# Kernel optimization log

Hardware: AMD Instinct MI355X
Metric: run time of the kernel (lower is better)

The kernel has to match this reference:

```python
import jax, jax.numpy as jnp
import numpy as np

B, T, I, H, D, C, OUT = 32, 128, 64, 256, 32, 64, 32
DECAY = 0.99

def _lin(k, fi, fo):
    lim = 1.0 / np.sqrt(fi)
    kw, kb = jax.random.split(k)
    W = jax.random.uniform(kw, (fi, fo), minval=-lim, maxval=lim, dtype=jnp.float32)
    b = jax.random.uniform(kb, (fo,), minval=-lim, maxval=lim, dtype=jnp.float32)
    return W, b

def setup_inputs():
    key = jax.random.key(0)
    ks = jax.random.split(key, 12)
    x = jax.random.normal(ks[0], (B, T, I), dtype=jnp.float32)
    lengths = jax.random.randint(ks[1], (B,), 1, T + 1)
    W_dg1, b_dg1 = _lin(ks[2], I + H, D)
    W_dg2, b_dg2 = _lin(ks[3], D, D)
    W_e1, b_e1 = _lin(ks[4], 2 * I, H)
    W_e2, b_e2 = _lin(ks[5], H, H)
    W_ih, b_ih = _lin(ks[6], H, 3 * H)
    W_hh, b_hh = _lin(ks[7], H, 3 * H)
    W_f1, b_f1 = _lin(ks[8], H, H)
    W_f2, b_f2 = _lin(ks[9], H, C)
    return dict(x=x, lengths=lengths, out_lengths=OUT,
                W_dg1=W_dg1, b_dg1=b_dg1, W_dg2=W_dg2, b_dg2=b_dg2,
                W_e1=W_e1, b_e1=b_e1, W_e2=W_e2, b_e2=b_e2,
                W_ih=W_ih, b_ih=b_ih, W_hh=W_hh, b_hh=b_hh,
                W_f1=W_f1, b_f1=b_f1, W_f2=W_f2, b_f2=b_f2)

def _forward(x, lengths, out_lengths, W_dg1, b_dg1, W_dg2, b_dg2, W_e1, b_e1, W_e2, b_e2,
             W_ih, b_ih, W_hh, b_hh, W_f1, b_f1, W_f2, b_f2):
    Bs, Ts, Is = x.shape
    Ds = W_dg2.shape[1]
    Hs = W_e2.shape[1]
    decay = DECAY ** jnp.arange(1, Ds + 1, dtype=x.dtype)  # [D]
    d_idx = jnp.arange(Ds)
    gkey = jax.random.key(42)
    g_enc = jax.random.gumbel(jax.random.fold_in(gkey, 0), (Ts, Bs, Ds), x.dtype)
    g_dec = jax.random.gumbel(jax.random.fold_in(gkey, 1), (out_lengths, Bs, Ds), x.dtype)
    masks = (jnp.arange(Ts)[None, :] < lengths[:, None]).astype(x.dtype)  # [B,T]

    def gumbel_softmax_hard(logits, g):
        # F.gumbel_softmax(..., tau=1.0, hard=True) straight-through estimator
        y_soft = jax.nn.softmax(logits + g, axis=-1)
        y_hard = jax.nn.one_hot(jnp.argmax(y_soft, axis=-1), Ds, dtype=logits.dtype)
        return y_hard + y_soft - jax.lax.stop_gradient(y_soft)

    def gru_cell(xin, h):
        # torch.nn.GRUCell gate order: r, z, n
        gi = xin @ W_ih + b_ih
        gh = h @ W_hh + b_hh
        i_r, i_z, i_n = jnp.split(gi, 3, axis=-1)
        h_r, h_z, h_n = jnp.split(gh, 3, axis=-1)
        r = jax.nn.sigmoid(i_r + h_r)
        z = jax.nn.sigmoid(i_z + h_z)
        n = jnp.tanh(i_n + r * h_n)
        return (1.0 - z) * n + z * h

    def step_core(buf, h, x_t, g_t, mem_t):
        cell_in = jnp.concatenate([x_t, h], axis=-1)
        logits = jax.nn.elu(cell_in @ W_dg1 + b_dg1) @ W_dg2 + b_dg2
        gate = gumbel_softmax_hard(logits, g_t)  # [B,D]
        # shift buffer along dim 1 (new[:, :-1] = old[:, 1:], last slot zeroed)
        new_buf = jnp.concatenate([buf[:, 1:], jnp.zeros_like(buf[:, :1])], axis=1)
        upd = x_t[:, None, :] * decay[None, :, None] * gate[:, :, None]  # [B,D,I]
        new_buf = new_buf.at[:, d_idx, d_idx].set(upd)  # diagonal scatter-assign
        rnn_in = jnp.concatenate([x_t, mem_t], axis=-1)
        rnn_in = jax.nn.elu(rnn_in @ W_e1 + b_e1) @ W_e2 + b_e2
        return new_buf, gru_cell(rnn_in, h)

    buf0 = jnp.zeros((Bs, Ds + 1, Ds, Is), x.dtype)
    h0 = jnp.zeros((Bs, Hs), x.dtype)

    def enc_step(carry, inp):
        buf, h = carry
        x_t, m_t, g_t = inp
        mem_t = buf[:, 0].sum(axis=1)  # [B,I]
        buf, nh = step_core(buf, h, x_t, g_t, mem_t)
        h = m_t[:, None] * nh + (1.0 - m_t[:, None]) * h
        return (buf, h), None

    (buf, h), _ = jax.lax.scan(enc_step, (buf0, h0),
                               (jnp.swapaxes(x, 0, 1), masks.T, g_enc))

    x_zero = jnp.zeros((Bs, Is), x.dtype)

    def dec_step(carry, g_t):
        buf, h = carry
        # get_current_memory(slide=True): roll -1 along dim1 with last slot zeroed
        buf = jnp.concatenate([buf[:, 1:], jnp.zeros_like(buf[:, :1])], axis=1)
        mem_t = buf[:, 0].sum(axis=1)
        buf, nh = step_core(buf, h, x_zero, g_t, mem_t)
        out = jax.nn.relu(nh @ W_f1 + b_f1) @ W_f2 + b_f2
        return (buf, nh), out

    _, outs = jax.lax.scan(dec_step, (buf, h), g_dec)  # [OUT,B,C]
    return jnp.swapaxes(outs, 0, 1)  # [B,OUT,C]

def reference(x, lengths, out_lengths, W_dg1, b_dg1, W_dg2, b_dg2, W_e1, b_e1, W_e2, b_e2,
              W_ih, b_ih, W_hh, b_hh, W_f1, b_f1, W_f2, b_f2):
    return _forward(x, lengths, out_lengths, W_dg1, b_dg1, W_dg2, b_dg2, W_e1, b_e1,
                    W_e2, b_e2, W_ih, b_ih, W_hh, b_hh, W_f1, b_f1, W_f2, b_f2)
```

## Files before the change

kernel.cpp:

```cpp
#include <hip/hip_runtime.h>
#include <math.h>


#define kB 32
#define kT 128
#define kI 64
#define kH 256
#define kD 32
#define kC 64
#define kOut 32
#define kSteps (kT + kOut)
#define NB 57
#define NTHR 256
#define NT_ALL (NB * NTHR)

#define WS_FL    384
#define WS_H     1856
#define WS_SEL   (WS_H + 4*8192)
#define WS_NZ    (WS_SEL + 128)
#define WS_W2    WS_NZ
#define WS_B2    (WS_W2 + kH*3*kH)
#define WS_G     (WS_B2 + 3*kH)
#define WS_P     (WS_G + kT*kB*kD)
#define WS_LINF  (WS_P + kT*kB*kH)
#define WS_O1    (WS_LINF + kSteps*kB*kH)
#define WS_ZERO_BYTES ((size_t)WS_NZ * sizeof(float))

__device__ __forceinline__ float cload(const float* p) {
  return __hip_atomic_load(p, __ATOMIC_RELAXED, __HIP_MEMORY_SCOPE_AGENT);
}
__device__ __forceinline__ void cstore(float* p, float v) {
  __hip_atomic_store(p, v, __ATOMIC_RELAXED, __HIP_MEMORY_SCOPE_AGENT);
}
__device__ __forceinline__ int cload_i(const int* p) {
  return __hip_atomic_load(p, __ATOMIC_RELAXED, __HIP_MEMORY_SCOPE_AGENT);
}
__device__ __forceinline__ void cstore_i(int* p, int v) {
  __hip_atomic_store(p, v, __ATOMIC_RELAXED, __HIP_MEMORY_SCOPE_AGENT);
}
__device__ __forceinline__ float4 cload4(const float* p) {
  float4 r;
  asm volatile("global_load_dwordx4 %0, %1, off sc0 sc1" : "=v"(r) : "v"(p));
  return r;
}
__device__ __forceinline__ void cstore4(float* p, float4 v) {
  cstore(p + 0, v.x); cstore(p + 1, v.y);
  cstore(p + 2, v.z); cstore(p + 3, v.w);
}
__device__ __forceinline__ void waitvm() {
  asm volatile("s_waitcnt vmcnt(0)" ::: "memory");
}

__device__ __forceinline__ void poll(const int* FL, int tid,
                                     int tH, int tD, int tS, int tF1, int tF2) {
  int thr;
  if      (tid < 32) thr = tH;
  else if (tid == 32) thr = tD;
  else if (tid == 33) thr = tS;
  else if (tid < 50) thr = tF1;
  else if (tid < 58) thr = tF2;
  else thr = 0;
  const int* p = FL + tid * 16;
  for (;;) {
    int ok = (thr <= 0) || (cload_i(p) >= thr);
    if (__syncthreads_count(ok) == NTHR) return;
    __builtin_amdgcn_s_sleep(2);
  }
}
__device__ __forceinline__ void setflag(int* FL, int tid, int idx, int val) {
  waitvm();
  __syncthreads();
  if (tid == 0) cstore_i(FL + idx * 16, val);
}

__device__ __forceinline__ void tf2x32(unsigned k0, unsigned k1,
                                       unsigned x0, unsigned x1,
                                       unsigned& o0, unsigned& o1) {
  unsigned ks2 = k0 ^ k1 ^ 0x1BD11BDAu;
  unsigned v0 = x0 + k0, v1 = x1 + k1;
#define TFR(r) { v0 += v1; v1 = (v1 << (r)) | (v1 >> (32-(r))); v1 ^= v0; }
  TFR(13) TFR(15) TFR(26) TFR(6)   v0 += k1;  v1 += ks2 + 1u;
  TFR(17) TFR(29) TFR(16) TFR(24)  v0 += ks2; v1 += k0  + 2u;
  TFR(13) TFR(15) TFR(26) TFR(6)   v0 += k0;  v1 += k1  + 3u;
  TFR(17) TFR(29) TFR(16) TFR(24)  v0 += k1;  v1 += ks2 + 4u;
  TFR(13) TFR(15) TFR(26) TFR(6)   v0 += ks2; v1 += k0  + 5u;
#undef TFR
  o0 = v0; o1 = v1;
}
__device__ __forceinline__ float bits_to_gumbel(unsigned bits) {
  float f = __uint_as_float((bits >> 9) | 0x3F800000u) - 1.0f;
  float u = f + 1.17549435e-38f;
  return -logf(-logf(u));
}

__device__ __forceinline__ void gridbar_full(unsigned* u, unsigned target) {
  __syncthreads();
  if (threadIdx.x == 0) {
    __threadfence();
    __hip_atomic_fetch_add(&u[320], 1u, __ATOMIC_ACQ_REL, __HIP_MEMORY_SCOPE_AGENT);
    while (__hip_atomic_load(&u[320], __ATOMIC_RELAXED, __HIP_MEMORY_SCOPE_AGENT) < target)
      __builtin_amdgcn_s_sleep(1);
    __threadfence();
  }
  __syncthreads();
}

__device__ __forceinline__ float elu1(float v) { return v > 0.f ? v : expm1f(v); }

__global__ __launch_bounds__(NTHR)
void delay_rnn(const float* __restrict__ x, const int* __restrict__ lengths,
               const float* __restrict__ W_dg1, const float* __restrict__ b_dg1,
               const float* __restrict__ W_dg2, const float* __restrict__ b_dg2,
               const float* __restrict__ W_e1,  const float* __restrict__ b_e1,
               const float* __restrict__ W_e2,  const float* __restrict__ b_e2,
               const float* __restrict__ W_ih,  const float* __restrict__ b_ih,
               const float* __restrict__ W_hh,  const float* __restrict__ b_hh,
               const float* __restrict__ W_f1,  const float* __restrict__ b_f1,
               const float* __restrict__ W_f2,  const float* __restrict__ b_f2,
               float* __restrict__ out, float* __restrict__ ws) {
  const int tid = threadIdx.x;
  const int bid = blockIdx.x;
  const int gid = bid * NTHR + tid;

  unsigned* baru = (unsigned*)ws;
  int*   FL    = (int*)(ws + WS_FL);
  float* hBuf  = ws + WS_H;
  int*   selG  = (int*)(ws + WS_SEL);
  float* W2g   = ws + WS_W2;
  float* B2g   = ws + WS_B2;
  float* g     = ws + WS_G;
  float* Pg    = ws + WS_P;
  float* linF  = ws + WS_LINF;
  float* o1B   = ws + WS_O1;

  __shared__ float S[35264];
  __shared__ float lgarr[1056];
  __shared__ float sb1[32], sb2[32], dec_sh[32];
  __shared__ int   sel[32], len_s[32], edest[32];

  {
    unsigned k0, k1;
    tf2x32(0u, 42u, 0u, 0u, k0, k1);
    for (int i = gid; i < kT * kB * kD; i += NT_ALL) {
      unsigned a, b;
      tf2x32(k0, k1, 0u, (unsigned)i, a, b);
      g[i] = bits_to_gumbel(a ^ b);
    }
  }
  for (int idx = gid; idx < kH * 3 * kH; idx += NT_ALL) {
    int k = idx / (3 * kH), n = idx % (3 * kH);
    const float* wr = W_e2 + k * kH;
    float s0 = 0, s1 = 0, s2 = 0, s3 = 0;
    for (int m = 0; m < kH; m += 4) {
      float4 wv = *(const float4*)(wr + m);
      s0 += wv.x * W_ih[(m    ) * 3 * kH + n];
      s1 += wv.y * W_ih[(m + 1) * 3 * kH + n];
      s2 += wv.z * W_ih[(m + 2) * 3 * kH + n];
      s3 += wv.w * W_ih[(m + 3) * 3 * kH + n];
    }
    W2g[idx] = ((s0 + s1) + (s2 + s3));
  }
  for (int n = gid; n < 3 * kH; n += NT_ALL) {
    float s = b_ih[n];
    for (int m = 0; m < kH; ++m) s += b_e2[m] * W_ih[m * 3 * kH + n];
    B2g[n] = s;
  }
  for (int idx = gid; idx < kT * kB * kH; idx += NT_ALL) {
    int s = idx >> 13, r = idx & 8191, b = r >> 8, j = r & 255;
    const float* xr = x + (b * kT + s) * kI;
    float a0 = 0, a1 = 0, a2 = 0, a3 = 0;
    for (int k = 0; k < 64; k += 4) {
      float4 xv = *(const float4*)(xr + k);
      a0 += xv.x * W_e1[(64 + k) * 256 + j];
      a1 += xv.y * W_e1[(65 + k) * 256 + j];
      a2 += xv.z * W_e1[(66 + k) * 256 + j];
      a3 += xv.w * W_e1[(67 + k) * 256 + j];
    }
    Pg[idx] = ((a0 + a1) + (a2 + a3));
  }
  for (int idx = gid; idx < kSteps * kB * kH; idx += NT_ALL) {
    int e = idx >> 13, r = idx & 8191, b = r >> 8, j = r & 255;
    float v = b_e1[j];
    if (e < kT) {
      const float* xr = x + (b * kT + e) * kI;
      float a0 = 0, a1 = 0, a2 = 0, a3 = 0;
      for (int k = 0; k < 64; k += 4) {
        float4 xv = *(const float4*)(xr + k);
        a0 += xv.x * W_e1[(k    ) * 256 + j];
        a1 += xv.y * W_e1[(k + 1) * 256 + j];
        a2 += xv.z * W_e1[(k + 2) * 256 + j];
        a3 += xv.w * W_e1[(k + 3) * 256 + j];
      }
      v += ((a0 + a1) + (a2 + a3));
    }
    linF[idx] = v;
  }

  gridbar_full(baru, NB);

  if (bid < 32) {
    float* whh = S; float* w2 = S + 6240;
    const int jb = bid * 8;
    for (int i = tid; i < 6144; i += NTHR) {
      int gg = i >> 11, r = i & 2047, jj = r >> 8, k = r & 255;
      whh[(gg * 8 + jj) * 260 + k] = W_hh[k * 768 + gg * 256 + jb + jj];
      w2 [(gg * 8 + jj) * 260 + k] = W2g [k * 768 + gg * 256 + jb + jj];
    }
    if (tid < 24) { int gg = tid / 8, jj = tid % 8;
      sb1[tid] = b_hh[gg * 256 + jb + jj];
      sb2[tid] = B2g [gg * 256 + jb + jj];
    }
    if (tid < 32) len_s[tid] = lengths[tid];
    __syncthreads();

    float* sH = S + 12480; float* sLin = S + 20800;
    float* red = S + 29120;
    for (int s = 0; s < kSteps; ++s) {
      int thrD = (s >= 2) ? ((s < kT) ? (s - 1) : kT) : 0;
      int thrS = (s >= 1) ? ((s < kT) ? s : kT) : 0;
      int tF1  = (s >= kT + 4) ? (s - 2) : 0;
      poll(FL, tid, s, thrD, thrS, tF1, 0);

      const float* hR = hBuf + (s & 3) * 8192;
      const float* lR = linF + s * 8192;
      const bool useC = (s >= 1 && s < kT);
      const float4* P4 = (const float4*)(Pg + (s - 1) * 8192);
      const int* selR = selG + ((s - 1) & 3) * 32;
      float4 th[8], tl[8], tp[8];
      int tsel[8];
      #pragma unroll
      for (int u8 = 0; u8 < 8; ++u8) {
        int i4 = (tid + u8 * 256) * 4;
        th[u8] = cload4(hR + i4);
        tl[u8] = cload4(lR + i4);
      }
      if (useC) {
        #pragma unroll
        for (int u8 = 0; u8 < 8; ++u8) {
          int idx = tid + u8 * 256; int b = idx >> 6, k4 = idx & 63;
          tp[u8] = P4[b * 64 + k4];
          tsel[u8] = cload_i(&selR[b]);
        }
      }
      waitvm();
      #pragma unroll
      for (int u8 = 0; u8 < 8; ++u8) {
        int idx = tid + u8 * 256; int b = idx >> 6, k4 = idx & 63;
        *(float4*)&sH[b * 260 + k4 * 4] = th[u8];
        float cx = 0.f, cy = 0.f, cz = 0.f, cw = 0.f;
        if (useC && tsel[u8] == 0) {
          cx = 0.99f * tp[u8].x; cy = 0.99f * tp[u8].y;
          cz = 0.99f * tp[u8].z; cw = 0.99f * tp[u8].w;
        }
        float4 v;
        v.x = elu1(tl[u8].x + cx);
        v.y = elu1(tl[u8].y + cy);
        v.z = elu1(tl[u8].z + cz);
        v.w = elu1(tl[u8].w + cw);
        *(float4*)&sLin[b * 260 + k4 * 4] = v;
      }
      __syncthreads();
      const float4* sH4 = (const float4*)sH;
      const float4* sL4 = (const float4*)sLin;
      const float4* wh4 = (const float4*)whh;
      const float4* w24 = (const float4*)w2;
      const int c  = tid & 7;
      const int b4 = (tid >> 3) & 7;
      const int kq = tid >> 6;
      float acc[24];
      #pragma unroll
      for (int a = 0; a < 24; ++a) acc[a] = 0.f;
      for (int kk = 0; kk < 16; ++kk) {
        int k4 = kq * 16 + kk;
        float4 wr[6];
        #pragma unroll
        for (int gg = 0; gg < 3; ++gg) {
          wr[gg]     = wh4[(gg * 8 + c) * 65 + k4];
          wr[3 + gg] = w24[(gg * 8 + c) * 65 + k4];
        }
        #pragma unroll
        for (int bi = 0; bi < 4; ++bi) {
          int b = bi * 8 + b4;
          float4 h4 = sH4[b * 65 + k4];
          float4 l4 = sL4[b * 65 + k4];
          #pragma unroll
          for (int gg = 0; gg < 3; ++gg) {
            float4 w = wr[gg];
            acc[bi * 6 + gg]     += h4.x * w.x + h4.y * w.y + h4.z * w.z + h4.w * w.w;
            w = wr[3 + gg];
            acc[bi * 6 + 3 + gg] += l4.x * w.x + l4.y * w.y + l4.z * w.z + l4.w * w.w;
          }
        }
      }
      #pragma unroll
      for (int bi = 0; bi < 4; ++bi)
        #pragma unroll
        for (int rr = 0; rr < 6; ++rr)
          red[kq * 1536 + rr * 256 + (bi * 8 + b4) * 8 + c] = acc[bi * 6 + rr];
      __syncthreads();
      {
        int b = tid >> 3, cc = tid & 7, jg = bid * 8 + cc;
        int lo = b * 8 + cc;
        float dots[6];
        #pragma unroll
        for (int rr = 0; rr < 6; ++rr)
          dots[rr] = (red[rr * 256 + lo] + red[1536 + rr * 256 + lo]) +
                     (red[3072 + rr * 256 + lo] + red[4608 + rr * 256 + lo]);
        float ghr = dots[0] + sb1[cc];
        float ghz = dots[1] + sb1[8 + cc];
        float ghn = dots[2] + sb1[16 + cc];
        float gir = dots[3] + sb2[cc];
        float giz = dots[4] + sb2[8 + cc];
        float gin = dots[5] + sb2[16 + cc];
        float r = 1.f / (1.f + expf(-(gir + ghr)));
        float z = 1.f / (1.f + expf(-(giz + ghz)));
        float n = tanhf(gin + r * ghn);
        float hold = sH[b * 260 + jg];
        float nh = (1.f - z) * n + z * hold;
        float hv = (s < kT) ? ((s < len_s[b]) ? nh : hold) : nh;
        cstore(&hBuf[((s + 1) & 3) * 8192 + b * 256 + jg], hv);
      }
      setflag(FL, tid, bid, s + 1);
    }
  }
  else if (bid == 32) {
    float* wdg1 = S; float* wdg2 = S + 10368;
    for (int i = tid; i < 10240; i += NTHR) {
      int j = i / 320, k = i % 320;
      wdg1[j * 324 + k] = W_dg1[k * 32 + j];
    }
    for (int i = tid; i < 1024; i += NTHR) wdg2[i] = W_dg2[i];
    if (tid < 32) { sb1[tid] = b_dg1[tid]; sb2[tid] = b_dg2[tid];
                    dec_sh[tid] = powf(0.99f, (float)(tid + 1)); }
    __syncthreads();

    float* sXH = S + 11392;
    float* red = S + 21760;
    float* l1s = S + 25856;
    for (int s = 0; s < kT; ++s) {
      poll(FL, tid, s, 0, 0, 0, 0);

      const float* hR = hBuf + (s & 3) * 8192;
      float4 th[8];
      #pragma unroll
      for (int u8 = 0; u8 < 8; ++u8) th[u8] = cload4(hR + (tid + u8 * 256) * 4);
      waitvm();
      #pragma unroll
      for (int u8 = 0; u8 < 8; ++u8) {
        int idx = tid + u8 * 256; int b = idx >> 6, k4 = idx & 63;
        *(float4*)&sXH[b * 324 + 64 + k4 * 4] = th[u8];
      }
      #pragma unroll
      for (int u2 = 0; u2 < 2; ++u2) {
        int idx = tid + u2 * 256; int b = idx >> 4, k4 = idx & 15;
        *(float4*)&sXH[b * 324 + k4 * 4] =
            *(const float4*)(x + (b * kT + s) * kI + k4 * 4);
      }
      __syncthreads();
      {
        const float4* sA4 = (const float4*)sXH;
        const float4* wd4 = (const float4*)wdg1;
        const int cq = tid & 7, b4 = (tid >> 3) & 7, kq = tid >> 6;
        float acc[16];
        #pragma unroll
        for (int a = 0; a < 16; ++a) acc[a] = 0.f;
        for (int kk = 0; kk < 20; ++kk) {
          int k4 = kq * 20 + kk;
          float4 wr[4];
          #pragma unroll
          for (int ci = 0; ci < 4; ++ci) wr[ci] = wd4[(cq * 4 + ci) * 81 + k4];
          #pragma unroll
          for (int bi = 0; bi < 4; ++bi) {
            float4 a4 = sA4[(bi * 8 + b4) * 81 + k4];
            #pragma unroll
            for (int ci = 0; ci < 4; ++ci) {
              float4 w = wr[ci];
              acc[bi * 4 + ci] += a4.x * w.x + a4.y * w.y + a4.z * w.z + a4.w * w.w;
            }
          }
        }
        #pragma unroll
        for (int bi = 0; bi < 4; ++bi)
          #pragma unroll
          for (int ci = 0; ci < 4; ++ci)
            red[kq * 1024 + (ci * 4 + bi) * 64 + cq * 8 + b4] = acc[bi * 4 + ci];
        __syncthreads();
        #pragma unroll
        for (int u4 = 0; u4 < 4; ++u4) {
          int o = tid * 4 + u4; int b = o >> 5, col = o & 31;
          int ci = col & 3, cq2 = col >> 2, bi = b >> 3, b42 = b & 7;
          int f = (ci * 4 + bi) * 64 + cq2 * 8 + b42;
          float v = (red[f] + red[1024 + f]) + (red[2048 + f] + red[3072 + f]);
          l1s[b * 36 + col] = elu1(v + sb1[col]);
        }
      }
      __syncthreads();
      for (int it = 0; it < 4; ++it) {
        int i = tid + it * 256; int b = i >> 5, j = i & 31;
        float sv = sb2[j];
        for (int k = 0; k < 32; ++k) sv += l1s[b * 36 + k] * wdg2[k * 32 + j];
        lgarr[b * 33 + j] = sv + g[(s * 32 + b) * 32 + j];
      }
      __syncthreads();
      if (tid < 32) {
        float best = lgarr[tid * 33]; int bi = 0;
        for (int j = 1; j < 32; ++j) {
          float v = lgarr[tid * 33 + j];
          if (v > best) { best = v; bi = j; }
        }
        sel[tid] = bi;
      }
      __syncthreads();
      if (tid < 32) cstore_i(&selG[(s & 3) * 32 + tid], sel[tid]);
      setflag(FL, tid, 33, s + 1);

      if (tid < 32) {
        int d = sel[tid], e = -1;
        if (d > 0) {
          int c = s + 1 + d;
          if (c < kT) e = c;
          else { int rr = c - kT - 1;
                 if (rr >= 0 && !(rr & 1)) {
                   int kk2 = rr >> 1; if (kk2 < kOut) e = kT + kk2; } }
        }
        edest[tid] = e;
      }
      __syncthreads();
      {
        float4 tv[8], tp2[8];
        int te[8], tb2[8];
        #pragma unroll
        for (int it = 0; it < 8; ++it) {
          int i = tid + it * 256; int b = i >> 6, q = i & 63;
          te[it] = edest[b]; tb2[it] = b;
          if (te[it] >= 0) {
            tv[it]  = cload4(linF + te[it] * 8192 + b * 256 + q * 4);
            tp2[it] = *(const float4*)(Pg + s * 8192 + b * 256 + q * 4);
          }
        }
        waitvm();
        #pragma unroll
        for (int it = 0; it < 8; ++it) {
          int i = tid + it * 256; int q = i & 63;
          if (te[it] >= 0) {
            float dec = dec_sh[sel[tb2[it]]];
            float4 v = tv[it], p = tp2[it];
            v.x += dec * p.x; v.y += dec * p.y;
            v.z += dec * p.z; v.w += dec * p.w;
            cstore4(linF + te[it] * 8192 + tb2[it] * 256 + q * 4, v);
          }
        }
      }
      setflag(FL, tid, 32, s + 1);
    }
  }
  else if (bid < 49) {
    float* wf1 = S;
    const int jb = (bid - 33) * 16;
    for (int i = tid; i < 4096; i += NTHR) {
      int jj = i >> 8, k = i & 255;
      wf1[jj * 260 + k] = W_f1[k * 256 + jb + jj];
    }
    if (tid < 16) sb1[tid] = b_f1[jb + tid];
    __syncthreads();

    float* sHf = S + 4160; float* red = S + 12480;
    for (int s = kT + 1; s <= kSteps; ++s) {
      int tF2 = (s >= kT + 5) ? (s - 2) : 0;
      poll(FL, tid, s, 0, 0, 0, tF2);

      const float* hR = hBuf + (s & 3) * 8192;
      float4 th[8];
      #pragma unroll
      for (int u8 = 0; u8 < 8; ++u8) th[u8] = cload4(hR + (tid + u8 * 256) * 4);
      waitvm();
      #pragma unroll
      for (int u8 = 0; u8 < 8; ++u8) {
        int idx = tid + u8 * 256; int b = idx >> 6, k4 = idx & 63;
        *(float4*)&sHf[b * 260 + k4 * 4] = th[u8];
      }
      __syncthreads();
      const float4* sH4 = (const float4*)sHf;
      const float4* w4p = (const float4*)wf1;
      const int cq = tid & 3, b4 = (tid >> 2) & 7, kq = tid >> 5;
      float acc[16];
      #pragma unroll
      for (int a = 0; a < 16; ++a) acc[a] = 0.f;
      for (int kk = 0; kk < 8; ++kk) {
        int k4 = kq * 8 + kk;
        float4 wr[4];
        #pragma unroll
        for (int ci = 0; ci < 4; ++ci) wr[ci] = w4p[(cq * 4 + ci) * 65 + k4];
        #pragma unroll
        for (int bi = 0; bi < 4; ++bi) {
          float4 h4 = sH4[(bi * 8 + b4) * 65 + k4];
          #pragma unroll
          for (int ci = 0; ci < 4; ++ci) {
            float4 w = wr[ci];
            acc[bi * 4 + ci] += h4.x * w.x + h4.y * w.y + h4.z * w.z + h4.w * w.w;
          }
        }
      }
      #pragma unroll
      for (int bi = 0; bi < 4; ++bi)
        #pragma unroll
        for (int ci = 0; ci < 4; ++ci)
          red[kq * 512 + (bi * 4 + ci) * 32 + cq * 8 + b4] = acc[bi * 4 + ci];
      __syncthreads();
      #pragma unroll
      for (int u2 = 0; u2 < 2; ++u2) {
        int o = tid * 2 + u2; int b = o >> 4, col = o & 15;
        int gg = ((b >> 3) * 4 + (col & 3)) * 32 + (col >> 2) * 8 + (b & 7);
        float v = 0.f;
        #pragma unroll
        for (int kq2 = 0; kq2 < 8; ++kq2) v += red[kq2 * 512 + gg];
        v += sb1[col];
        cstore(&o1B[(s & 3) * 8192 + b * 256 + (bid - 33) * 16 + col],
               v > 0.f ? v : 0.f);
      }
      __syncthreads();
      setflag(FL, tid, bid + 1, s + 1);
    }
  }
  else {
    float* wf2 = S;
    const int cb = (bid - 49) * 8;
    for (int i = tid; i < 2048; i += NTHR) {
      int cc = i >> 8, k = i & 255;
      wf2[cc * 260 + k] = W_f2[k * 64 + cb + cc];
    }
    if (tid < 8) sb2[tid] = b_f2[cb + tid];
    __syncthreads();

    float* sO = S + 2080; float* red = S + 10400;
    for (int s = kT + 2; s <= kSteps + 1; ++s) {
      poll(FL, tid, 0, 0, 0, s, 0);

      const float* oR = o1B + ((s - 1) & 3) * 8192;
      float4 to[8];
      #pragma unroll
      for (int u8 = 0; u8 < 8; ++u8) to[u8] = cload4(oR + (tid + u8 * 256) * 4);
      waitvm();
      #pragma unroll
      for (int u8 = 0; u8 < 8; ++u8) {
        int idx = tid + u8 * 256; int b = idx >> 6, k4 = idx & 63;
        *(float4*)&sO[b * 260 + k4 * 4] = to[u8];
      }
      __syncthreads();
      const float4* sO4 = (const float4*)sO;
      const float4* w4p = (const float4*)wf2;
      const int c = tid & 7, b4 = (tid >> 3) & 7, kq = tid >> 6;
      float acc[4] = {0.f, 0.f, 0.f, 0.f};
      for (int kk = 0; kk < 16; ++kk) {
        int k4 = kq * 16 + kk;
        float4 w = w4p[c * 65 + k4];
        #pragma unroll
        for (int bi = 0; bi < 4; ++bi) {
          float4 o4 = sO4[(bi * 8 + b4) * 65 + k4];
          acc[bi] += o4.x * w.x + o4.y * w.y + o4.z * w.z + o4.w * w.w;
        }
      }
      #pragma unroll
      for (int bi = 0; bi < 4; ++bi)
        red[kq * 256 + bi * 64 + b4 * 8 + c] = acc[bi];
      __syncthreads();
      { int b = tid >> 3, col = tid & 7;
        int gg = (b >> 3) * 64 + (b & 7) * 8 + col;
        float v = (red[gg] + red[256 + gg]) + (red[512 + gg] + red[768 + gg]);
        out[(b * kOut + (s - 2 - kT)) * kC + (bid - 49) * 8 + col] =
            v + sb2[col];
      }
      __syncthreads();
      setflag(FL, tid, bid + 1, s + 1);
    }
  }
}

extern "C" void kernel_launch(void* const* d_in, const int* in_sizes, int n_in,
                              void* d_out, int out_size, void* d_ws, size_t ws_size,
                              hipStream_t stream) {
  (void)in_sizes; (void)n_in; (void)out_size; (void)ws_size;
  const float* x      = (const float*)d_in[0];
  const int*   lens   = (const int*)  d_in[1];
  const float* W_dg1  = (const float*)d_in[3];
  const float* b_dg1  = (const float*)d_in[4];
  const float* W_dg2  = (const float*)d_in[5];
  const float* b_dg2  = (const float*)d_in[6];
  const float* W_e1   = (const float*)d_in[7];
  const float* b_e1   = (const float*)d_in[8];
  const float* W_e2   = (const float*)d_in[9];
  const float* b_e2   = (const float*)d_in[10];
  const float* W_ih   = (const float*)d_in[11];
  const float* b_ih   = (const float*)d_in[12];
  const float* W_hh   = (const float*)d_in[13];
  const float* b_hh   = (const float*)d_in[14];
  const float* W_f1   = (const float*)d_in[15];
  const float* b_f1   = (const float*)d_in[16];
  const float* W_f2   = (const float*)d_in[17];
  const float* b_f2   = (const float*)d_in[18];

  hipMemsetAsync(d_ws, 0, WS_ZERO_BYTES, stream);
  delay_rnn<<<dim3(NB), dim3(NTHR), 0, stream>>>(
      x, lens, W_dg1, b_dg1, W_dg2, b_dg2, W_e1, b_e1, W_e2, b_e2,
      W_ih, b_ih, W_hh, b_hh, W_f1, b_f1, W_f2, b_f2,
      (float*)d_out, (float*)d_ws);
}
```

Baseline: 2.251 ms.

## Merge dispatch flags, vectorize coherent stores, prefetch x before polling

The separate selection flag and delay-gate flag are merged into one, so the recurrent blocks poll one fewer flag and the flag indices of the later stage blocks shift down by one. The h and FC1 outputs are staged in shared memory and written as 128-bit coherent stores instead of scalar atomic stores. The x row is loaded before the poll spin so its latency overlaps the wait. This aims to cut per-step synchronization and store latency on the serial critical path, at the cost of an extra syncthreads per step and some loss of overlap for consumers that used to start on the earlier selection flag.

```diff
diff --git a/kernel.cpp b/kernel.cpp
--- a/kernel.cpp
+++ b/kernel.cpp
@@ -26,6 +26,8 @@
 #define WS_O1    (WS_LINF + kSteps*kB*kH)
 #define WS_ZERO_BYTES ((size_t)WS_NZ * sizeof(float))
 
+typedef float f32x4v __attribute__((ext_vector_type(4)));
+
 __device__ __forceinline__ float cload(const float* p) {
   return __hip_atomic_load(p, __ATOMIC_RELAXED, __HIP_MEMORY_SCOPE_AGENT);
 }
@@ -43,22 +45,21 @@
   asm volatile("global_load_dwordx4 %0, %1, off sc0 sc1" : "=v"(r) : "v"(p));
   return r;
 }
-__device__ __forceinline__ void cstore4(float* p, float4 v) {
-  cstore(p + 0, v.x); cstore(p + 1, v.y);
-  cstore(p + 2, v.z); cstore(p + 3, v.w);
+__device__ __forceinline__ void cstore4w(float* p, float4 v) {
+  f32x4v t; t.x = v.x; t.y = v.y; t.z = v.z; t.w = v.w;
+  asm volatile("global_store_dwordx4 %0, %1, off sc0 sc1" :: "v"(p), "v"(t) : "memory");
 }
 __device__ __forceinline__ void waitvm() {
   asm volatile("s_waitcnt vmcnt(0)" ::: "memory");
 }
 
 __device__ __forceinline__ void poll(const int* FL, int tid,
-                                     int tH, int tD, int tS, int tF1, int tF2) {
+                                     int tH, int tDG, int tF1, int tF2) {
   int thr;
   if      (tid < 32) thr = tH;
-  else if (tid == 32) thr = tD;
-  else if (tid == 33) thr = tS;
-  else if (tid < 50) thr = tF1;
-  else if (tid < 58) thr = tF2;
+  else if (tid == 32) thr = tDG;
+  else if (tid < 49) thr = tF1;
+  else if (tid < 57) thr = tF2;
   else thr = 0;
   const int* p = FL + tid * 16;
   for (;;) {
@@ -133,8 +134,7 @@
   float* linF  = ws + WS_LINF;
   float* o1B   = ws + WS_O1;
 
-  __shared__ float S[35264];
-  __shared__ float lgarr[1056];
+  __shared__ float S[35520];
   __shared__ float sb1[32], sb2[32], dec_sh[32];
   __shared__ int   sel[32], len_s[32], edest[32];
 
@@ -215,11 +215,11 @@
 
     float* sH = S + 12480; float* sLin = S + 20800;
     float* red = S + 29120;
+    float* hstage = S + 35264;
     for (int s = 0; s < kSteps; ++s) {
-      int thrD = (s >= 2) ? ((s < kT) ? (s - 1) : kT) : 0;
-      int thrS = (s >= 1) ? ((s < kT) ? s : kT) : 0;
-      int tF1  = (s >= kT + 4) ? (s - 2) : 0;
-      poll(FL, tid, s, thrD, thrS, tF1, 0);
+      int tDG = (s >= 1) ? (s < kT ? s : kT) : 0;
+      int tF1 = (s >= kT + 4) ? (s - 2) : 0;
+      poll(FL, tid, s, tDG, tF1, 0);
 
       const float* hR = hBuf + (s & 3) * 8192;
       const float* lR = linF + s * 8192;
@@ -299,7 +299,7 @@
           red[kq * 1536 + rr * 256 + (bi * 8 + b4) * 8 + c] = acc[bi * 6 + rr];
       __syncthreads();
       {
-        int b = tid >> 3, cc = tid & 7, jg = bid * 8 + cc;
+        int b = tid >> 3, cc = tid & 7, jg = jb + cc;
         int lo = b * 8 + cc;
         float dots[6];
         #pragma unroll
@@ -318,7 +318,13 @@
         float hold = sH[b * 260 + jg];
         float nh = (1.f - z) * n + z * hold;
         float hv = (s < kT) ? ((s < len_s[b]) ? nh : hold) : nh;
-        cstore(&hBuf[((s + 1) & 3) * 8192 + b * 256 + jg], hv);
+        hstage[b * 8 + cc] = hv;
+      }
+      __syncthreads();
+      if (tid < 64) {
+        int b = tid >> 1, q = tid & 1;
+        float4 h4 = *(const float4*)&hstage[b * 8 + q * 4];
+        cstore4w(&hBuf[((s + 1) & 3) * 8192 + b * 256 + jb + q * 4], h4);
       }
       setflag(FL, tid, bid, s + 1);
     }
@@ -337,8 +343,15 @@
     float* sXH = S + 11392;
     float* red = S + 21760;
     float* l1s = S + 25856;
+    float* lg  = S + 27008;
     for (int s = 0; s < kT; ++s) {
-      poll(FL, tid, s, 0, 0, 0, 0);
+      float4 tx[2];
+      #pragma unroll
+      for (int u2 = 0; u2 < 2; ++u2) {
+        int idx = tid + u2 * 256; int b = idx >> 4, k4 = idx & 15;
+        tx[u2] = *(const float4*)(x + (b * kT + s) * kI + k4 * 4);
+      }
+      poll(FL, tid, s, 0, 0, 0);
 
       const float* hR = hBuf + (s & 3) * 8192;
       float4 th[8];
@@ -353,8 +366,7 @@
       #pragma unroll
       for (int u2 = 0; u2 < 2; ++u2) {
         int idx = tid + u2 * 256; int b = idx >> 4, k4 = idx & 15;
-        *(float4*)&sXH[b * 324 + k4 * 4] =
-            *(const float4*)(x + (b * kT + s) * kI + k4 * 4);
+        *(float4*)&sXH[b * 324 + k4 * 4] = tx[u2];
       }
       __syncthreads();
       {
@@ -399,22 +411,20 @@
         int i = tid + it * 256; int b = i >> 5, j = i & 31;
         float sv = sb2[j];
         for (int k = 0; k < 32; ++k) sv += l1s[b * 36 + k] * wdg2[k * 32 + j];
-        lgarr[b * 33 + j] = sv + g[(s * 32 + b) * 32 + j];
+        lg[b * 33 + j] = sv + g[(s * 32 + b) * 32 + j];
       }
       __syncthreads();
       if (tid < 32) {
-        float best = lgarr[tid * 33]; int bi = 0;
+        float best = lg[tid * 33]; int bi = 0;
         for (int j = 1; j < 32; ++j) {
-          float v = lgarr[tid * 33 + j];
+          float v = lg[tid * 33 + j];
           if (v > best) { best = v; bi = j; }
         }
         sel[tid] = bi;
       }
       __syncthreads();
-      if (tid < 32) cstore_i(&selG[(s & 3) * 32 + tid], sel[tid]);
-      setflag(FL, tid, 33, s + 1);
-
       if (tid < 32) {
+        cstore_i(&selG[(s & 3) * 32 + tid], sel[tid]);
         int d = sel[tid], e = -1;
         if (d > 0) {
           int c = s + 1 + d;
@@ -447,7 +457,7 @@
             float4 v = tv[it], p = tp2[it];
             v.x += dec * p.x; v.y += dec * p.y;
             v.z += dec * p.z; v.w += dec * p.w;
-            cstore4(linF + te[it] * 8192 + tb2[it] * 256 + q * 4, v);
+            cstore4w(linF + te[it] * 8192 + tb2[it] * 256 + q * 4, v);
           }
         }
       }
@@ -465,9 +475,10 @@
     __syncthreads();
 
     float* sHf = S + 4160; float* red = S + 12480;
+    float* ostage = S + 16576;
     for (int s = kT + 1; s <= kSteps; ++s) {
       int tF2 = (s >= kT + 5) ? (s - 2) : 0;
-      poll(FL, tid, s, 0, 0, 0, tF2);
+      poll(FL, tid, s, 0, 0, tF2);
 
       const float* hR = hBuf + (s & 3) * 8192;
       float4 th[8];
@@ -515,11 +526,15 @@
         #pragma unroll
         for (int kq2 = 0; kq2 < 8; ++kq2) v += red[kq2 * 512 + gg];
         v += sb1[col];
-        cstore(&o1B[(s & 3) * 8192 + b * 256 + (bid - 33) * 16 + col],
-               v > 0.f ? v : 0.f);
-      }
-      __syncthreads();
-      setflag(FL, tid, bid + 1, s + 1);
+        ostage[b * 16 + col] = v > 0.f ? v : 0.f;
+      }
+      __syncthreads();
+      if (tid < 128) {
+        int b = tid >> 2, q = tid & 3;
+        float4 o4 = *(const float4*)&ostage[b * 16 + q * 4];
+        cstore4w(&o1B[(s & 3) * 8192 + b * 256 + jb + q * 4], o4);
+      }
+      setflag(FL, tid, bid, s + 1);
     }
   }
   else {
@@ -534,7 +549,7 @@
 
     float* sO = S + 2080; float* red = S + 10400;
     for (int s = kT + 2; s <= kSteps + 1; ++s) {
-      poll(FL, tid, 0, 0, 0, s, 0);
+      poll(FL, tid, 0, 0, s, 0);
 
       const float* oR = o1B + ((s - 1) & 3) * 8192;
       float4 to[8];
@@ -567,11 +582,10 @@
       { int b = tid >> 3, col = tid & 7;
         int gg = (b >> 3) * 64 + (b & 7) * 8 + col;
         float v = (red[gg] + red[256 + gg]) + (red[512 + gg] + red[768 + gg]);
-        out[(b * kOut + (s - 2 - kT)) * kC + (bid - 49) * 8 + col] =
-            v + sb2[col];
-      }
-      __syncthreads();
-      setflag(FL, tid, bid + 1, s + 1);
+        out[(b * kOut + (s - 2 - kT)) * kC + cb + col] = v + sb2[col];
+      }
+      __syncthreads();
+      setflag(FL, tid, bid, s + 1);
     }
   }
 }
```

Measured after the change: 2.192 ms. -2.6%, faster.
